# Kernel tuning notes

Measured on AMD Instinct MI355X. Metric: run time of the kernel, lower is better.

The kernel has to match this reference:

```python
import jax, jax.numpy as jnp
from jax import lax
import numpy as np

B, S = 8, 256
V, E, P, H = 50257, 512, 768, 1000  # vocab, word emb, paragraph dim, lstm hidden


def setup_inputs() -> dict:
    key = jax.random.key(0)
    ks = iter(jax.random.split(key, 40))
    s = 1.0 / np.sqrt(H)
    u = lambda shape: jax.random.uniform(next(ks), shape, jnp.float32, -s, s)
    inp = {}
    inp["x"] = jax.random.randint(next(ks), (B, S), 0, V)
    inp["emb_word"] = jax.random.normal(next(ks), (V, E), jnp.float32)
    inp["enc_emb"] = jax.random.normal(next(ks), (V, P), jnp.float32)  # encoder stub table
    # lstm1: 2-layer unidirectional, gate order i,f,g,o; single fused bias (b_ih+b_hh)
    inp["l1_Wih0"], inp["l1_Whh0"], inp["l1_b0"] = u((4 * H, E)), u((4 * H, H)), u((4 * H,))
    inp["l1_Wih1"], inp["l1_Whh1"], inp["l1_b1"] = u((4 * H, H)), u((4 * H, H)), u((4 * H,))
    # lstm2: 2-layer bidirectional (f=forward dir, r=reverse dir); layer1 input is 2H
    inp["l2f_Wih0"], inp["l2f_Whh0"], inp["l2f_b0"] = u((4 * H, P)), u((4 * H, H)), u((4 * H,))
    inp["l2r_Wih0"], inp["l2r_Whh0"], inp["l2r_b0"] = u((4 * H, P)), u((4 * H, H)), u((4 * H,))
    inp["l2f_Wih1"], inp["l2f_Whh1"], inp["l2f_b1"] = u((4 * H, 2 * H)), u((4 * H, H)), u((4 * H,))
    inp["l2r_Wih1"], inp["l2r_Whh1"], inp["l2r_b1"] = u((4 * H, 2 * H)), u((4 * H, H)), u((4 * H,))
    inp["w1"], inp["b1"] = u((1, H)), u((1,))
    inp["w2"], inp["b2"] = u((1, 2 * H)), u((1,))
    inp["wc"], inp["bc"] = u((1, 2)), u((1,))
    return inp


def lstm_layer(xs, Wih, Whh, b, reverse=False):
    # xs: [B,S,D] -> hs: [B,S,H]. Input-to-gate GEMM hoisted out of the scan.
    xg = jnp.einsum("bsd,gd->bsg", xs, Wih) + b  # [B,S,4H]
    if reverse:
        xg = xg[:, ::-1]
    h0 = jnp.zeros((xs.shape[0], Whh.shape[1]), xs.dtype)

    def step(carry, xt):
        h, c = carry
        g = xt + h @ Whh.T
        i, f, gg, o = jnp.split(g, 4, axis=-1)
        c = jax.nn.sigmoid(f) * c + jax.nn.sigmoid(i) * jnp.tanh(gg)
        h = jax.nn.sigmoid(o) * jnp.tanh(c)
        return (h, c), h

    _, hs = lax.scan(step, (h0, h0), jnp.swapaxes(xg, 0, 1))
    hs = jnp.swapaxes(hs, 0, 1)
    return hs[:, ::-1] if reverse else hs


def bilstm_layer(xs, Wf, Uf, bf, Wr, Ur, br):
    return jnp.concatenate(
        [lstm_layer(xs, Wf, Uf, bf, False), lstm_layer(xs, Wr, Ur, br, True)], -1
    )


def reference(x, emb_word, enc_emb,
              l1_Wih0, l1_Whh0, l1_b0, l1_Wih1, l1_Whh1, l1_b1,
              l2f_Wih0, l2f_Whh0, l2f_b0, l2r_Wih0, l2r_Whh0, l2r_b0,
              l2f_Wih1, l2f_Whh1, l2f_b1, l2r_Wih1, l2r_Whh1, l2r_b1,
              w1, b1, w2, b2, wc, bc):
    # paragraph branch: encoder stub -> 2-layer biLSTM -> last step -> linear2
    p = enc_emb[x]  # [B,S,P]
    p = bilstm_layer(p, l2f_Wih0, l2f_Whh0, l2f_b0, l2r_Wih0, l2r_Whh0, l2r_b0)
    p = bilstm_layer(p, l2f_Wih1, l2f_Whh1, l2f_b1, l2r_Wih1, l2r_Whh1, l2r_b1)
    paragraph_scores = p[:, -1] @ w2.T + b2  # [B,1]
    # word branch: embedding -> 2-layer LSTM -> last step -> linear1
    w = emb_word[x]  # [B,S,E]
    w = lstm_layer(w, l1_Wih0, l1_Whh0, l1_b0)
    w = lstm_layer(w, l1_Wih1, l1_Whh1, l1_b1)
    word_scores = w[:, -1] @ w1.T + b1  # [B,1]
    combo = jnp.concatenate([paragraph_scores, word_scores], -1)  # [B,2]
    return combo @ wc.T + bc  # [B,1]
```

## Files before the change

### kernel.cpp

```cpp
#include <hip/hip_runtime.h>
#include <stdint.h>
#include <math.h>


typedef __attribute__((ext_vector_type(8))) short short8;
typedef __attribute__((ext_vector_type(4))) float f32x4;
typedef __attribute__((ext_vector_type(4))) unsigned int u32x4;
typedef unsigned long long ull;

#define BB 8
#define SS 256
#define MM (BB*SS)
#define HH 1000
#define GG 4000
#define NP 4096
#define HP 1024

__device__ __forceinline__ unsigned short f2bf(float f){
  unsigned u = __builtin_bit_cast(unsigned, f);
  unsigned r = u + 0x7fffu + ((u >> 16) & 1u);
  return (unsigned short)(r >> 16);
}
__device__ __forceinline__ float bf2f(unsigned short s){
  unsigned u = ((unsigned)s) << 16;
  return __builtin_bit_cast(float, u);
}
__device__ __forceinline__ float sigf(float x){ return 1.0f / (1.0f + expf(-x)); }
__device__ __forceinline__ float fsig(float x){ return 1.0f / (1.0f + __expf(-x)); }
__device__ __forceinline__ float ftanh(float x){
  const float e = __expf(-2.0f * fabsf(x));
  const float r = (1.0f - e) / (1.0f + e);
  return x < 0.0f ? -r : r;
}
__device__ __forceinline__ bool valid4(ull v){
  return (v & 0xffffull) && (v & 0xffff0000ull) &&
         (v & 0xffff00000000ull) && (v >> 48);
}

__device__ __forceinline__ void async_copy16(const void* g, void* l){
  __builtin_amdgcn_global_load_lds(
      (const __attribute__((address_space(1))) unsigned int*)g,
      (__attribute__((address_space(3))) unsigned int*)l, 16, 0, 0);
}

__global__ void kzero(unsigned int* __restrict__ p, size_t nwords){
  size_t stride = (size_t)gridDim.x * blockDim.x;
  for (size_t i = (size_t)blockIdx.x*blockDim.x + threadIdx.x; i < nwords; i += stride)
    p[i] = 0u;
}

__global__ void kpadw(const float* __restrict__ src, unsigned short* __restrict__ dst,
                      int K, int Kpad){
  size_t total = (size_t)NP * Kpad;
  size_t stride = (size_t)gridDim.x * blockDim.x;
  for (size_t i = (size_t)blockIdx.x*blockDim.x + threadIdx.x; i < total; i += stride){
    int nrow = (int)(i / Kpad);
    int k    = (int)(i % Kpad);
    float v = (nrow < GG && k < K) ? src[(size_t)nrow*K + k] : 0.0f;
    dst[i] = f2bf(v);
  }
}

__global__ void kgather(const float* __restrict__ emb, const int* __restrict__ x,
                        unsigned short* __restrict__ dst, int E){
  size_t total = (size_t)MM * E;
  size_t stride = (size_t)gridDim.x * blockDim.x;
  for (size_t i = (size_t)blockIdx.x*blockDim.x + threadIdx.x; i < total; i += stride){
    size_t m = i / E, e = i % E;
    dst[i] = f2bf(emb[(size_t)x[m]*E + e]);
  }
}

__global__ void kdecode(ull* __restrict__ p, size_t n64){
  size_t stride = (size_t)gridDim.x * blockDim.x;
  for (size_t i = (size_t)blockIdx.x*blockDim.x + threadIdx.x; i < n64; i += stride){
    const ull v = p[i];
    ull m = 0;
    if (v & 0xffffull)          m |= 0xffffull;
    if (v & 0xffff0000ull)      m |= 0xffff0000ull;
    if (v & 0xffff00000000ull)  m |= 0xffff00000000ull;
    if (v >> 48)                m |= 0xffff000000000000ull;
    p[i] = (~v) & m;
  }
}

__launch_bounds__(256, 2)
__global__ void kgemm(const unsigned short* __restrict__ A,
                      const unsigned short* __restrict__ W,
                      const float* __restrict__ bias,
                      float* __restrict__ out, int Kpad){
  __shared__ __align__(16) unsigned short ldsA[128*64];
  __shared__ __align__(16) unsigned short ldsB[128*64];
  const int tid = threadIdx.x;
  const int w = tid >> 6, l = tid & 63;
  const int wr = w >> 1, wc = w & 1;
  const int tm = blockIdx.x & 15, tn = blockIdx.x >> 4;
  const size_t Kb = (size_t)Kpad * 2;
  const int nk = Kpad >> 6;

  f32x4 acc[4][4];
#pragma unroll
  for (int a = 0; a < 4; ++a)
#pragma unroll
    for (int b = 0; b < 4; ++b) acc[a][b] = (f32x4){0.f,0.f,0.f,0.f};

  for (int kt = 0; kt < nk; ++kt){
#pragma unroll
    for (int c = 0; c < 4; ++c){
      const int chunk = c*4 + w;
      const int flat = chunk*1024 + l*16;
      const int row = flat >> 7;
      const int off = flat & 127;
      const int soff = off ^ ((row & 7) << 4);
      async_copy16((const char*)A + (size_t)(tm*128+row)*Kb + (size_t)kt*128 + soff,
                   (char*)ldsA + chunk*1024);
      async_copy16((const char*)W + (size_t)(tn*128+row)*Kb + (size_t)kt*128 + soff,
                   (char*)ldsB + chunk*1024);
    }
    asm volatile("s_waitcnt vmcnt(0)" ::: "memory");
    __syncthreads();

#pragma unroll
    for (int ks = 0; ks < 2; ++ks){
      short8 af[4], bf[4];
#pragma unroll
      for (int mf = 0; mf < 4; ++mf){
        const int row = wr*64 + mf*16 + (l & 15);
        const int off = ((ks*32 + (l>>4)*8)*2) ^ ((row & 7) << 4);
        af[mf] = *(const short8*)((const char*)ldsA + row*128 + off);
      }
#pragma unroll
      for (int nf = 0; nf < 4; ++nf){
        const int row = wc*64 + nf*16 + (l & 15);
        const int off = ((ks*32 + (l>>4)*8)*2) ^ ((row & 7) << 4);
        bf[nf] = *(const short8*)((const char*)ldsB + row*128 + off);
      }
#pragma unroll
      for (int mf = 0; mf < 4; ++mf)
#pragma unroll
        for (int nf = 0; nf < 4; ++nf)
          acc[mf][nf] = __builtin_amdgcn_mfma_f32_16x16x32_bf16(
              af[mf], bf[nf], acc[mf][nf], 0, 0, 0);
    }
    __syncthreads();
  }

#pragma unroll
  for (int nf = 0; nf < 4; ++nf){
    const int n = tn*128 + wc*64 + nf*16 + (l & 15);
    if (n < GG){
      const float bv = bias[n];
#pragma unroll
      for (int mf = 0; mf < 4; ++mf){
#pragma unroll
        for (int q = 0; q < 4; ++q){
          const int m = tm*128 + wr*64 + mf*16 + (l>>4)*4 + q;
          out[(size_t)m*GG + n] = acc[mf][nf][q] + bv;
        }
      }
    }
  }
}

struct LstmDesc {
  const float* xg;
  const float* whh;
  unsigned short* hbuf;
  int hstride;
  int joff;
  int rev;
};
struct ScanArgs {
  LstmDesc d[3];
};

__launch_bounds__(512, 2)
__global__ void kscan(ScanArgs args){
  __shared__ __align__(16) unsigned short h_lds[2][8][HP];
  __shared__ float ex[8][128];
  __shared__ unsigned short exh[8][32];
  const int tid = threadIdx.x;
  const int wv = tid >> 6, l = tid & 63;
  const int lstm = blockIdx.x >> 5, slice = blockIdx.x & 31;
  const LstmDesc D = args.d[lstm];

  const int col = l & 15, g4 = l >> 4;
  const int gate = col >> 2, jl = col & 3;
  const int j = slice*32 + wv*4 + jl;
  const int n = gate*HH + j;
  const bool jv = (j < HH);

  short8 wf[32];
#pragma unroll
  for (int ks = 0; ks < 32; ++ks){
    short8 v = (short8){0,0,0,0,0,0,0,0};
    const int kb = ks*32 + g4*8;
    if (jv && kb < HH){
      const float* s = D.whh + (size_t)n*HH + kb;
#pragma unroll
      for (int i = 0; i < 8; ++i) v[i] = (short)f2bf(s[i]);
    }
    wf[ks] = v;
  }

  int chr_[4], coff_[4], ldso_[4];
  bool cneed_[4];
#pragma unroll
  for (int cc = 0; cc < 4; ++cc){
    const int fb = (cc*512 + tid) * 8;
    chr_[cc]  = fb >> 11;
    coff_[cc] = fb & 2047;
    cneed_[cc] = (coff_[cc] < 2000);
    ldso_[cc] = chr_[cc]*2048 + (coff_[cc] ^ ((chr_[cc] & 7) << 4));
  }

  const int arow = l & 15;
  const bool av = arow < 8;
  const int aswz = (arow & 7) << 4;
  float c_reg = 0.f;
  const int ub = l & 7, ujl = (l >> 3) & 3;
  const int ubase = slice*32 + wv*4;
  const bool sv = (ubase < HH);

  float xgv[4] = {0.f,0.f,0.f,0.f};
  {
    const int pos0 = D.rev ? (SS-1) : 0;
    if (g4 < 2 && jv){
#pragma unroll
      for (int q = 0; q < 4; ++q)
        xgv[q] = D.xg[(size_t)((g4*4+q)*SS + pos0)*GG + n];
    }
  }

  for (int t = 0; t < SS; ++t){
    const int pos  = D.rev ? (SS-1 - t) : t;
    const int ppos = D.rev ? (pos + 1) : (pos - 1);
    const int buf = t & 1;

    ull val[4] = {0ull, 0ull, 0ull, 0ull};
    if (t > 0){
      const char* src_[4];
      unsigned pend = 0;
#pragma unroll
      for (int cc = 0; cc < 4; ++cc){
        src_[cc] = (const char*)D.hbuf
            + ((size_t)(chr_[cc]*SS + ppos)*D.hstride + D.joff)*2 + coff_[cc];
        if (cneed_[cc]) pend |= 1u << cc;
      }
      while (pend){
        ull tmp[4];
#pragma unroll
        for (int cc = 0; cc < 4; ++cc)
          if (pend & (1u << cc))
            tmp[cc] = __hip_atomic_load((const ull*)src_[cc],
                                        __ATOMIC_RELAXED, __HIP_MEMORY_SCOPE_AGENT);
#pragma unroll
        for (int cc = 0; cc < 4; ++cc)
          if ((pend & (1u << cc)) && valid4(tmp[cc])){
            val[cc] = ~tmp[cc];
            pend &= ~(1u << cc);
          }
      }
    }
#pragma unroll
    for (int cc = 0; cc < 4; ++cc)
      *(ull*)((char*)h_lds + buf*16384 + ldso_[cc]) = val[cc];
    __syncthreads();

    const char* abase = (const char*)h_lds + buf*16384 + arow*2048;
    f32x4 a0 = (f32x4){0.f,0.f,0.f,0.f};
    f32x4 a1 = (f32x4){0.f,0.f,0.f,0.f};
#pragma unroll
    for (int ks = 0; ks < 16; ++ks){
      const int off0 = (((2*ks  )*64) | (g4*16)) ^ aswz;
      const int off1 = (((2*ks+1)*64) | (g4*16)) ^ aswz;
      short8 s0 = av ? *(const short8*)(abase + off0) : (short8){0,0,0,0,0,0,0,0};
      short8 s1 = av ? *(const short8*)(abase + off1) : (short8){0,0,0,0,0,0,0,0};
      a0 = __builtin_amdgcn_mfma_f32_16x16x32_bf16(s0, wf[2*ks  ], a0, 0, 0, 0);
      a1 = __builtin_amdgcn_mfma_f32_16x16x32_bf16(s1, wf[2*ks+1], a1, 0, 0, 0);
    }

    if (g4 < 2){
#pragma unroll
      for (int q = 0; q < 4; ++q)
        ex[wv][(jl*4 + gate)*8 + (g4*4 + q)] = a0[q] + a1[q] + xgv[q];
    }

    if (l < 32){
      const float iv = ex[wv][(ujl*4 + 0)*8 + ub];
      const float fv = ex[wv][(ujl*4 + 1)*8 + ub];
      const float gv = ex[wv][(ujl*4 + 2)*8 + ub];
      const float ov = ex[wv][(ujl*4 + 3)*8 + ub];
      c_reg = fsig(fv)*c_reg + fsig(iv)*ftanh(gv);
      const float h = fsig(ov)*ftanh(c_reg);
      exh[wv][ub*4 + ujl] = f2bf(h);
    }
    if (l < 8 && sv){
      const ull hv = ~(*(const ull*)&exh[wv][l*4]);
      ull* dst = (ull*)&D.hbuf[(size_t)(l*SS + pos)*D.hstride + D.joff + ubase];
      __hip_atomic_store(dst, hv, __ATOMIC_RELAXED, __HIP_MEMORY_SCOPE_AGENT);
    }

    float xgn[4] = {0.f,0.f,0.f,0.f};
    if (t+1 < SS && g4 < 2 && jv){
      const int npos = D.rev ? (pos - 1) : (pos + 1);
#pragma unroll
      for (int q = 0; q < 4; ++q)
        xgn[q] = D.xg[(size_t)((g4*4+q)*SS + npos)*GG + n];
    }
#pragma unroll
    for (int q = 0; q < 4; ++q) xgv[q] = xgn[q];
  }
}

__global__ void kfinal(const unsigned short* __restrict__ hw1,
                       const unsigned short* __restrict__ hpf1,
                       const float* __restrict__ xgr1,
                       const float* __restrict__ w1, const float* __restrict__ b1,
                       const float* __restrict__ w2, const float* __restrict__ b2,
                       const float* __restrict__ wc, const float* __restrict__ bc,
                       float* __restrict__ out){
  __shared__ float red[256];
  const int tid = threadIdx.x;
  for (int b = 0; b < BB; ++b){
    const size_t r = (size_t)(b*SS + (SS-1));
    float ps = 0.f, wsm = 0.f;
    for (int j = tid; j < HH; j += 256){
      unsigned short hp = hpf1[r*1024 + j];
      unsigned short hw = hw1 [r*1024 + j];
      hp = hp ? (unsigned short)~hp : (unsigned short)0;
      hw = hw ? (unsigned short)~hw : (unsigned short)0;
      ps  += bf2f(hp) * w2[j];
      const float iv = xgr1[r*GG + j];
      const float gv = xgr1[r*GG + 2000 + j];
      const float ov = xgr1[r*GG + 3000 + j];
      const float cc = sigf(iv)*tanhf(gv);
      ps  += sigf(ov)*tanhf(cc) * w2[HH + j];
      wsm += bf2f(hw) * w1[j];
    }
    red[tid] = ps; __syncthreads();
    for (int s = 128; s > 0; s >>= 1){ if (tid < s) red[tid] += red[tid+s]; __syncthreads(); }
    const float PS = red[0]; __syncthreads();
    red[tid] = wsm; __syncthreads();
    for (int s = 128; s > 0; s >>= 1){ if (tid < s) red[tid] += red[tid+s]; __syncthreads(); }
    const float WS = red[0]; __syncthreads();
    if (tid == 0)
      out[b] = wc[0]*(PS + b2[0]) + wc[1]*(WS + b1[0]) + bc[0];
    __syncthreads();
  }
}

extern "C" void kernel_launch(void* const* d_in, const int* in_sizes, int n_in,
                              void* d_out, int out_size, void* d_ws, size_t ws_size,
                              hipStream_t stream){
  const int*   x      = (const int*)  d_in[0];
  const float* embw   = (const float*)d_in[1];
  const float* embp   = (const float*)d_in[2];
  const float* l1Wih0 = (const float*)d_in[3];
  const float* l1Whh0 = (const float*)d_in[4];
  const float* l1b0   = (const float*)d_in[5];
  const float* l1Wih1 = (const float*)d_in[6];
  const float* l1Whh1 = (const float*)d_in[7];
  const float* l1b1   = (const float*)d_in[8];
  const float* f0Wih  = (const float*)d_in[9];
  const float* f0Whh  = (const float*)d_in[10];
  const float* f0b    = (const float*)d_in[11];
  const float* r0Wih  = (const float*)d_in[12];
  const float* r0Whh  = (const float*)d_in[13];
  const float* r0b    = (const float*)d_in[14];
  const float* f1Wih  = (const float*)d_in[15];
  const float* f1Whh  = (const float*)d_in[16];
  const float* f1b    = (const float*)d_in[17];
  const float* r1Wih  = (const float*)d_in[18];
  const float* r1Whh  = (const float*)d_in[19];
  const float* r1b    = (const float*)d_in[20];
  const float* w1     = (const float*)d_in[21];
  const float* b1     = (const float*)d_in[22];
  const float* w2     = (const float*)d_in[23];
  const float* b2     = (const float*)d_in[24];
  const float* wc     = (const float*)d_in[25];
  const float* bc     = (const float*)d_in[26];
  float* out = (float*)d_out;
  (void)in_sizes; (void)n_in; (void)out_size; (void)ws_size;

  char* ws = (char*)d_ws;
  size_t off = 0;
  auto alloc = [&](size_t bytes)->char*{
    char* p = ws + off;
    off += (bytes + 255) & ~(size_t)255;
    return p;
  };
  unsigned short* pw_l1Wih0 = (unsigned short*)alloc((size_t)NP*512*2);
  unsigned short* pw_f0Wih  = (unsigned short*)alloc((size_t)NP*768*2);
  unsigned short* pw_r0Wih  = (unsigned short*)alloc((size_t)NP*768*2);
  unsigned short* pw_l1Wih1 = (unsigned short*)alloc((size_t)NP*1024*2);
  unsigned short* pw_f1Wih  = (unsigned short*)alloc((size_t)NP*2048*2);
  unsigned short* pw_r1Wih  = (unsigned short*)alloc((size_t)NP*2048*2);
  unsigned short* a_w = (unsigned short*)alloc((size_t)MM*512*2);
  unsigned short* a_p = (unsigned short*)alloc((size_t)MM*768*2);
  float* xg0 = (float*)alloc((size_t)MM*GG*4);
  float* xg1 = (float*)alloc((size_t)MM*GG*4);
  float* xg2 = (float*)alloc((size_t)MM*GG*4);
  char* zbase = ws + off;
  unsigned short* h_w0  = (unsigned short*)alloc((size_t)MM*1024*2);
  unsigned short* cat0  = (unsigned short*)alloc((size_t)MM*2048*2);
  unsigned short* h_w1  = (unsigned short*)alloc((size_t)MM*1024*2);
  unsigned short* h_pf1 = (unsigned short*)alloc((size_t)MM*1024*2);
  size_t zwords = (size_t)((ws + off) - zbase) / 4;

  kzero<<<dim3(1024), dim3(256), 0, stream>>>((unsigned int*)zbase, zwords);
  kpadw<<<dim3(1024), dim3(256), 0, stream>>>(l1Wih0, pw_l1Wih0, 512, 512);
  kpadw<<<dim3(1024), dim3(256), 0, stream>>>(f0Wih,  pw_f0Wih,  768, 768);
  kpadw<<<dim3(1024), dim3(256), 0, stream>>>(r0Wih,  pw_r0Wih,  768, 768);
  kpadw<<<dim3(1024), dim3(256), 0, stream>>>(l1Wih1, pw_l1Wih1, 1000, 1024);
  kpadw<<<dim3(1024), dim3(256), 0, stream>>>(f1Wih,  pw_f1Wih,  2000, 2048);
  kpadw<<<dim3(1024), dim3(256), 0, stream>>>(r1Wih,  pw_r1Wih,  2000, 2048);
  kgather<<<dim3(512), dim3(256), 0, stream>>>(embw, x, a_w, 512);
  kgather<<<dim3(512), dim3(256), 0, stream>>>(embp, x, a_p, 768);

  kgemm<<<dim3(512), dim3(256), 0, stream>>>(a_w, pw_l1Wih0, l1b0, xg0, 512);
  kgemm<<<dim3(512), dim3(256), 0, stream>>>(a_p, pw_f0Wih,  f0b,  xg1, 768);
  kgemm<<<dim3(512), dim3(256), 0, stream>>>(a_p, pw_r0Wih,  r0b,  xg2, 768);

  {
    ScanArgs sa;
    sa.d[0] = LstmDesc{xg0, l1Whh0, h_w0, 1024, 0, 0};
    sa.d[1] = LstmDesc{xg1, f0Whh,  cat0, 2048, 0, 0};
    sa.d[2] = LstmDesc{xg2, r0Whh,  cat0, 2048, 1000, 1};
    kscan<<<dim3(96), dim3(512), 0, stream>>>(sa);
  }

  kdecode<<<dim3(2048), dim3(256), 0, stream>>>(
      (ull*)h_w0, ((size_t)MM*1024 + (size_t)MM*2048) / 4);

  kgemm<<<dim3(512), dim3(256), 0, stream>>>(h_w0, pw_l1Wih1, l1b1, xg0, 1024);
  kgemm<<<dim3(512), dim3(256), 0, stream>>>(cat0, pw_f1Wih,  f1b,  xg1, 2048);
  kgemm<<<dim3(512), dim3(256), 0, stream>>>(cat0, pw_r1Wih,  r1b,  xg2, 2048);

  {
    ScanArgs sa;
    sa.d[0] = LstmDesc{xg0, l1Whh1, h_w1,  1024, 0, 0};
    sa.d[1] = LstmDesc{xg1, f1Whh,  h_pf1, 1024, 0, 0};
    sa.d[2] = LstmDesc{nullptr, nullptr, nullptr, 1024, 0, 0};
    kscan<<<dim3(64), dim3(512), 0, stream>>>(sa);
  }

  kfinal<<<dim3(1), dim3(256), 0, stream>>>(h_w1, h_pf1, xg2,
                                            w1, b1, w2, b2, wc, bc, out);
}
```

Measured before the change: 2.185 ms.

## Pin each LSTM scan to one XCD and poll hidden state with wide cache-bypassing loads

```diff
diff --git a/kernel.cpp b/kernel.cpp
--- a/kernel.cpp
+++ b/kernel.cpp
@@ -32,10 +32,18 @@
   const float r = (1.0f - e) / (1.0f + e);
   return x < 0.0f ? -r : r;
 }
-__device__ __forceinline__ bool valid4(ull v){
-  return (v & 0xffffull) && (v & 0xffff0000ull) &&
-         (v & 0xffff00000000ull) && (v >> 48);
-}
+__device__ __forceinline__ bool ok8(u32x4 v){
+  return (v[0] & 0xffffu) && (v[0] >> 16) && (v[1] & 0xffffu) && (v[1] >> 16) &&
+         (v[2] & 0xffffu) && (v[2] >> 16) && (v[3] & 0xffffu) && (v[3] >> 16);
+}
+__device__ __forceinline__ u32x4 inv4(u32x4 v){
+  return (u32x4){~v[0], ~v[1], ~v[2], ~v[3]};
+}
+
+#define LD16_L2(dst, addr) \
+  asm volatile("global_load_dwordx4 %0, %1, off sc0" : "=v"(dst) : "v"(addr))
+#define LD16_L3(dst, addr) \
+  asm volatile("global_load_dwordx4 %0, %1, off sc0 sc1" : "=v"(dst) : "v"(addr))
 
 __device__ __forceinline__ void async_copy16(const void* g, void* l){
   __builtin_amdgcn_global_load_lds(
@@ -175,13 +183,15 @@
 };
 
 __launch_bounds__(512, 2)
-__global__ void kscan(ScanArgs args){
+__global__ void kscan(ScanArgs args, int nl){
   __shared__ __align__(16) unsigned short h_lds[2][8][HP];
   __shared__ float ex[8][128];
   __shared__ unsigned short exh[8][32];
+  const int xcd = blockIdx.x & 7;
+  if (xcd >= nl) return;
   const int tid = threadIdx.x;
   const int wv = tid >> 6, l = tid & 63;
-  const int lstm = blockIdx.x >> 5, slice = blockIdx.x & 31;
+  const int lstm = xcd, slice = blockIdx.x >> 3;
   const LstmDesc D = args.d[lstm];
 
   const int col = l & 15, g4 = l >> 4;
@@ -203,16 +213,14 @@
     wf[ks] = v;
   }
 
-  int chr_[4], coff_[4], ldso_[4];
-  bool cneed_[4];
-#pragma unroll
-  for (int cc = 0; cc < 4; ++cc){
-    const int fb = (cc*512 + tid) * 8;
-    chr_[cc]  = fb >> 11;
-    coff_[cc] = fb & 2047;
-    cneed_[cc] = (coff_[cc] < 2000);
-    ldso_[cc] = chr_[cc]*2048 + (coff_[cc] ^ ((chr_[cc] & 7) << 4));
-  }
+  const int fb0 = tid*16, fb1 = (512 + tid)*16;
+  const int hr0 = fb0 >> 11, off0 = fb0 & 2047;
+  const int hr1 = fb1 >> 11, off1 = fb1 & 2047;
+  const bool need0 = off0 < 2000, need1 = off1 < 2000;
+  const int ldso0 = hr0*2048 + (off0 ^ ((hr0 & 7) << 4));
+  const int ldso1 = hr1*2048 + (off1 ^ ((hr1 & 7) << 4));
+  const size_t gb0 = ((size_t)hr0*SS*D.hstride + D.joff)*2 + off0;
+  const size_t gb1 = ((size_t)hr1*SS*D.hstride + D.joff)*2 + off1;
 
   const int arow = l & 15;
   const bool av = arow < 8;
@@ -237,34 +245,24 @@
     const int ppos = D.rev ? (pos + 1) : (pos - 1);
     const int buf = t & 1;
 
-    ull val[4] = {0ull, 0ull, 0ull, 0ull};
+    u32x4 v0r = (u32x4){0u,0u,0u,0u}, v1r = (u32x4){0u,0u,0u,0u};
     if (t > 0){
-      const char* src_[4];
-      unsigned pend = 0;
-#pragma unroll
-      for (int cc = 0; cc < 4; ++cc){
-        src_[cc] = (const char*)D.hbuf
-            + ((size_t)(chr_[cc]*SS + ppos)*D.hstride + D.joff)*2 + coff_[cc];
-        if (cneed_[cc]) pend |= 1u << cc;
+      const char* g0 = (const char*)D.hbuf + gb0 + (size_t)ppos*D.hstride*2;
+      const char* g1 = (const char*)D.hbuf + gb1 + (size_t)ppos*D.hstride*2;
+      unsigned pend = (need0 ? 1u : 0u) | (need1 ? 2u : 0u);
+      u32x4 r0 = (u32x4){0u,0u,0u,0u}, r1 = (u32x4){0u,0u,0u,0u};
+      int it = 0;
+      while (pend){
+        const bool slow = ((++it) & 3) == 0;
+        if (pend & 1u){ if (slow) LD16_L3(r0, g0); else LD16_L2(r0, g0); }
+        if (pend & 2u){ if (slow) LD16_L3(r1, g1); else LD16_L2(r1, g1); }
+        asm volatile("s_waitcnt vmcnt(0)" ::: "memory");
+        if ((pend & 1u) && ok8(r0)){ v0r = inv4(r0); pend &= ~1u; }
+        if ((pend & 2u) && ok8(r1)){ v1r = inv4(r1); pend &= ~2u; }
       }
-      while (pend){
-        ull tmp[4];
-#pragma unroll
-        for (int cc = 0; cc < 4; ++cc)
-          if (pend & (1u << cc))
-            tmp[cc] = __hip_atomic_load((const ull*)src_[cc],
-                                        __ATOMIC_RELAXED, __HIP_MEMORY_SCOPE_AGENT);
-#pragma unroll
-        for (int cc = 0; cc < 4; ++cc)
-          if ((pend & (1u << cc)) && valid4(tmp[cc])){
-            val[cc] = ~tmp[cc];
-            pend &= ~(1u << cc);
-          }
-      }
-    }
-#pragma unroll
-    for (int cc = 0; cc < 4; ++cc)
-      *(ull*)((char*)h_lds + buf*16384 + ldso_[cc]) = val[cc];
+    }
+    *(u32x4*)((char*)h_lds + buf*16384 + ldso0) = v0r;
+    *(u32x4*)((char*)h_lds + buf*16384 + ldso1) = v1r;
     __syncthreads();
 
     const char* abase = (const char*)h_lds + buf*16384 + arow*2048;
@@ -272,10 +270,10 @@
     f32x4 a1 = (f32x4){0.f,0.f,0.f,0.f};
 #pragma unroll
     for (int ks = 0; ks < 16; ++ks){
-      const int off0 = (((2*ks  )*64) | (g4*16)) ^ aswz;
-      const int off1 = (((2*ks+1)*64) | (g4*16)) ^ aswz;
-      short8 s0 = av ? *(const short8*)(abase + off0) : (short8){0,0,0,0,0,0,0,0};
-      short8 s1 = av ? *(const short8*)(abase + off1) : (short8){0,0,0,0,0,0,0,0};
+      const int o0 = (((2*ks  )*64) | (g4*16)) ^ aswz;
+      const int o1 = (((2*ks+1)*64) | (g4*16)) ^ aswz;
+      short8 s0 = av ? *(const short8*)(abase + o0) : (short8){0,0,0,0,0,0,0,0};
+      short8 s1 = av ? *(const short8*)(abase + o1) : (short8){0,0,0,0,0,0,0,0};
       a0 = __builtin_amdgcn_mfma_f32_16x16x32_bf16(s0, wf[2*ks  ], a0, 0, 0, 0);
       a1 = __builtin_amdgcn_mfma_f32_16x16x32_bf16(s1, wf[2*ks+1], a1, 0, 0, 0);
     }
@@ -298,6 +296,7 @@
     if (l < 8 && sv){
       const ull hv = ~(*(const ull*)&exh[wv][l*4]);
       ull* dst = (ull*)&D.hbuf[(size_t)(l*SS + pos)*D.hstride + D.joff + ubase];
+      asm volatile("global_store_dwordx2 %0, %1, off" :: "v"(dst), "v"(hv) : "memory");
       __hip_atomic_store(dst, hv, __ATOMIC_RELAXED, __HIP_MEMORY_SCOPE_AGENT);
     }
 
@@ -427,7 +426,7 @@
     sa.d[0] = LstmDesc{xg0, l1Whh0, h_w0, 1024, 0, 0};
     sa.d[1] = LstmDesc{xg1, f0Whh,  cat0, 2048, 0, 0};
     sa.d[2] = LstmDesc{xg2, r0Whh,  cat0, 2048, 1000, 1};
-    kscan<<<dim3(96), dim3(512), 0, stream>>>(sa);
+    kscan<<<dim3(256), dim3(512), 0, stream>>>(sa, 3);
   }
 
   kdecode<<<dim3(2048), dim3(256), 0, stream>>>(
@@ -442,7 +441,7 @@
     sa.d[0] = LstmDesc{xg0, l1Whh1, h_w1,  1024, 0, 0};
     sa.d[1] = LstmDesc{xg1, f1Whh,  h_pf1, 1024, 0, 0};
     sa.d[2] = LstmDesc{nullptr, nullptr, nullptr, 1024, 0, 0};
-    kscan<<<dim3(64), dim3(512), 0, stream>>>(sa);
+    kscan<<<dim3(256), dim3(512), 0, stream>>>(sa, 2);
   }
 
   kfinal<<<dim3(1), dim3(256), 0, stream>>>(h_w1, h_pf1, xg2,
```

After: 6.796 ms. 3.11x slower.

## Pin each LSTM scan to one XCD via runtime workgroup assignment

Applied to the files above, without the earlier changes.

```diff
diff --git a/kernel.cpp b/kernel.cpp
--- a/kernel.cpp
+++ b/kernel.cpp
@@ -172,6 +172,9 @@
 };
 struct ScanArgs {
   LstmDesc d[3];
+  unsigned int* asg;
+  int nl;
+  int nwg;
 };
 
 __launch_bounds__(512, 2)
@@ -179,11 +182,44 @@
   __shared__ __align__(16) unsigned short h_lds[2][8][HP];
   __shared__ float ex[8][128];
   __shared__ unsigned short exh[8][32];
+  __shared__ int s_lstm, s_slice;
   const int tid = threadIdx.x;
+
+  if (tid == 0){
+    unsigned xcc = 0;
+    asm volatile("s_getreg_b32 %0, hwreg(HW_REG_XCC_ID)" : "=s"(xcc));
+    xcc &= 7u;
+    int lstm = -1, slice = -1;
+    const unsigned r = __hip_atomic_fetch_add(&args.asg[xcc], 1u,
+                          __ATOMIC_RELAXED, __HIP_MEMORY_SCOPE_AGENT);
+    asm volatile("s_waitcnt vmcnt(0)" ::: "memory");
+    if ((int)xcc < args.nl && r < 32u){ lstm = (int)xcc; slice = (int)r; }
+    __hip_atomic_fetch_add(&args.asg[8], 1u,
+                           __ATOMIC_RELAXED, __HIP_MEMORY_SCOPE_AGENT);
+    while (__hip_atomic_load(&args.asg[8], __ATOMIC_RELAXED,
+                             __HIP_MEMORY_SCOPE_AGENT) < (unsigned)args.nwg)
+      __builtin_amdgcn_s_sleep(1);
+    if (lstm < 0){
+      unsigned s = __hip_atomic_fetch_add(&args.asg[9], 1u,
+                      __ATOMIC_RELAXED, __HIP_MEMORY_SCOPE_AGENT);
+      asm volatile("s_waitcnt vmcnt(0)" ::: "memory");
+      for (int ll = 0; ll < args.nl; ++ll){
+        unsigned c = __hip_atomic_load(&args.asg[ll], __ATOMIC_RELAXED,
+                                       __HIP_MEMORY_SCOPE_AGENT);
+        const unsigned cl = c < 32u ? c : 32u;
+        const unsigned un = 32u - cl;
+        if (s < un){ lstm = ll; slice = (int)(cl + s); break; }
+        s -= un;
+      }
+    }
+    s_lstm = lstm; s_slice = slice;
+  }
+  __syncthreads();
+  const int lstm = s_lstm, slice = s_slice;
+  if (lstm < 0) return;
+  const LstmDesc D = args.d[lstm];
+
   const int wv = tid >> 6, l = tid & 63;
-  const int lstm = blockIdx.x >> 5, slice = blockIdx.x & 31;
-  const LstmDesc D = args.d[lstm];
-
   const int col = l & 15, g4 = l >> 4;
   const int gate = col >> 2, jl = col & 3;
   const int j = slice*32 + wv*4 + jl;
@@ -252,8 +288,22 @@
 #pragma unroll
         for (int cc = 0; cc < 4; ++cc)
           if (pend & (1u << cc))
-            tmp[cc] = __hip_atomic_load((const ull*)src_[cc],
-                                        __ATOMIC_RELAXED, __HIP_MEMORY_SCOPE_AGENT);
+            asm volatile("global_load_dwordx2 %0, %1, off sc0"
+                         : "=v"(tmp[cc]) : "v"(src_[cc]) : "memory");
+        asm volatile("s_waitcnt vmcnt(0)" ::: "memory");
+#pragma unroll
+        for (int cc = 0; cc < 4; ++cc)
+          if ((pend & (1u << cc)) && valid4(tmp[cc])){
+            val[cc] = ~tmp[cc];
+            pend &= ~(1u << cc);
+          }
+        if (!pend) break;
+#pragma unroll
+        for (int cc = 0; cc < 4; ++cc)
+          if (pend & (1u << cc))
+            asm volatile("global_load_dwordx2 %0, %1, off sc0 sc1"
+                         : "=v"(tmp[cc]) : "v"(src_[cc]) : "memory");
+        asm volatile("s_waitcnt vmcnt(0)" ::: "memory");
 #pragma unroll
         for (int cc = 0; cc < 4; ++cc)
           if ((pend & (1u << cc)) && valid4(tmp[cc])){
@@ -272,10 +322,10 @@
     f32x4 a1 = (f32x4){0.f,0.f,0.f,0.f};
 #pragma unroll
     for (int ks = 0; ks < 16; ++ks){
-      const int off0 = (((2*ks  )*64) | (g4*16)) ^ aswz;
-      const int off1 = (((2*ks+1)*64) | (g4*16)) ^ aswz;
-      short8 s0 = av ? *(const short8*)(abase + off0) : (short8){0,0,0,0,0,0,0,0};
-      short8 s1 = av ? *(const short8*)(abase + off1) : (short8){0,0,0,0,0,0,0,0};
+      const int o0 = (((2*ks  )*64) | (g4*16)) ^ aswz;
+      const int o1 = (((2*ks+1)*64) | (g4*16)) ^ aswz;
+      short8 s0 = av ? *(const short8*)(abase + o0) : (short8){0,0,0,0,0,0,0,0};
+      short8 s1 = av ? *(const short8*)(abase + o1) : (short8){0,0,0,0,0,0,0,0};
       a0 = __builtin_amdgcn_mfma_f32_16x16x32_bf16(s0, wf[2*ks  ], a0, 0, 0, 0);
       a1 = __builtin_amdgcn_mfma_f32_16x16x32_bf16(s1, wf[2*ks+1], a1, 0, 0, 0);
     }
@@ -298,7 +348,9 @@
     if (l < 8 && sv){
       const ull hv = ~(*(const ull*)&exh[wv][l*4]);
       ull* dst = (ull*)&D.hbuf[(size_t)(l*SS + pos)*D.hstride + D.joff + ubase];
-      __hip_atomic_store(dst, hv, __ATOMIC_RELAXED, __HIP_MEMORY_SCOPE_AGENT);
+      asm volatile("global_store_dwordx2 %0, %1, off sc0 sc1\n\t"
+                   "global_store_dwordx2 %0, %1, off"
+                   :: "v"(dst), "v"(hv) : "memory");
     }
 
     float xgn[4] = {0.f,0.f,0.f,0.f};
@@ -406,6 +458,8 @@
   unsigned short* cat0  = (unsigned short*)alloc((size_t)MM*2048*2);
   unsigned short* h_w1  = (unsigned short*)alloc((size_t)MM*1024*2);
   unsigned short* h_pf1 = (unsigned short*)alloc((size_t)MM*1024*2);
+  unsigned int* asgB = (unsigned int*)alloc(16*4);
+  unsigned int* asgD = (unsigned int*)alloc(16*4);
   size_t zwords = (size_t)((ws + off) - zbase) / 4;
 
   kzero<<<dim3(1024), dim3(256), 0, stream>>>((unsigned int*)zbase, zwords);
@@ -427,7 +481,8 @@
     sa.d[0] = LstmDesc{xg0, l1Whh0, h_w0, 1024, 0, 0};
     sa.d[1] = LstmDesc{xg1, f0Whh,  cat0, 2048, 0, 0};
     sa.d[2] = LstmDesc{xg2, r0Whh,  cat0, 2048, 1000, 1};
-    kscan<<<dim3(96), dim3(512), 0, stream>>>(sa);
+    sa.asg = asgB; sa.nl = 3; sa.nwg = 256;
+    kscan<<<dim3(256), dim3(512), 0, stream>>>(sa);
   }
 
   kdecode<<<dim3(2048), dim3(256), 0, stream>>>(
@@ -442,7 +497,8 @@
     sa.d[0] = LstmDesc{xg0, l1Whh1, h_w1,  1024, 0, 0};
     sa.d[1] = LstmDesc{xg1, f1Whh,  h_pf1, 1024, 0, 0};
     sa.d[2] = LstmDesc{nullptr, nullptr, nullptr, 1024, 0, 0};
-    kscan<<<dim3(64), dim3(512), 0, stream>>>(sa);
+    sa.asg = asgD; sa.nl = 2; sa.nwg = 256;
+    kscan<<<dim3(256), dim3(512), 0, stream>>>(sa);
   }
 
   kfinal<<<dim3(1), dim3(256), 0, stream>>>(h_w1, h_pf1, xg2,
```

New measurement: 6.994 ms. +220.1%, slower.
